# Kernel tuning notes

Hardware: AMD Instinct MI355X
Metric: run time of the kernel (lower is better)

Reference implementation:

```python
import jax, jax.numpy as jnp
import numpy as np

B, T = 64, 2048
ENC, DEC = 512, 1024
CONV, K, HID = 32, 31, 256
PAD = (K - 1) // 2


def setup_inputs() -> dict:
    key = jax.random.key(0)
    ks = jax.random.split(key, 10)
    s = 0.05
    enc_output = jax.random.normal(ks[0], (B, T, ENC), jnp.float32)
    dec_state = jax.random.normal(ks[1], (B, DEC), jnp.float32)
    prev = jax.random.uniform(ks[2], (B, T), jnp.float32)
    prev_att_w = prev / jnp.sum(prev, axis=-1, keepdims=True)
    text_len = jax.random.randint(ks[3], (B,), T // 2, T + 1)
    W_enc = jax.random.normal(ks[4], (HID, ENC), jnp.float32) * s
    b_enc = jnp.zeros((HID,), jnp.float32)
    W_dec = jax.random.normal(ks[5], (HID, DEC), jnp.float32) * s
    W_att = jax.random.normal(ks[6], (HID, CONV), jnp.float32) * s
    conv_w = jax.random.normal(ks[7], (CONV, 1, K), jnp.float32) * s  # (out,in,k)
    w_w = jax.random.normal(ks[8], (1, HID), jnp.float32) * s
    w_b = jnp.zeros((1,), jnp.float32)
    return dict(enc_output=enc_output, dec_state=dec_state, prev_att_w=prev_att_w,
                text_len=text_len, W_enc=W_enc, b_enc=b_enc, W_dec=W_dec,
                W_att=W_att, conv_w=conv_w, w_w=w_w, w_b=w_b)


def reference(enc_output, dec_state, prev_att_w, text_len,
              W_enc, b_enc, W_dec, W_att, conv_w, w_w, w_b):
    # pad mask: True where position is beyond the valid length
    mask = jnp.arange(T)[None, :] >= text_len[:, None]              # (B,T) bool

    # processed_memory = fc_enc(enc_output)
    pm = jnp.einsum('btc,hc->bth', enc_output, W_enc) + b_enc       # (B,T,HID)

    # location conv over previous attention weights (same-padding 1D conv)
    conv = jax.lax.conv_general_dilated(
        prev_att_w[:, None, :], conv_w, window_strides=(1,),
        padding=[(PAD, PAD)], dimension_numbers=('NCH', 'OIH', 'NCH'))  # (B,CONV,T)
    att_conv = jnp.einsum('bct,hc->bth', conv, W_att)               # (B,T,HID)

    dec = (dec_state @ W_dec.T)[:, None, :]                         # (B,1,HID)

    energy = jnp.einsum('bth,oh->bto', jnp.tanh(att_conv + pm + dec), w_w)[..., 0] + w_b[0]
    energy = jnp.where(mask, -jnp.inf, energy)                      # masked fill
    att_w = jax.nn.softmax(energy, axis=1)                          # (B,T)
    att_c = jnp.einsum('btc,bt->bc', enc_output, att_w)             # (B,ENC)
    return att_c, att_w
```

## Files before the change

### kernel.cpp

```cpp
#include <hip/hip_runtime.h>
#include <hip/hip_bf16.h>

#define NB   64
#define NT   2048
#define NENC 512
#define NDEC 1024
#define NCONV 32
#define NK   31
#define NHID 256
#define NPAD 15

typedef __attribute__((ext_vector_type(8))) short bf16x8;
typedef __attribute__((ext_vector_type(4))) float f32x4;

#define WS_WSW 0
#define WS_GSW 262144
#define WS_DEC 278528

__device__ __forceinline__ short f2b(float f) {
  unsigned u = __builtin_bit_cast(unsigned, f);
  u += 0x7FFFu + ((u >> 16) & 1u);
  return (short)(u >> 16);
}

__global__ __launch_bounds__(256) void prep_kernel(
    const float* __restrict__ W_enc, const float* __restrict__ W_att,
    const float* __restrict__ conv_w, const float* __restrict__ dec_state,
    const float* __restrict__ W_dec, char* __restrict__ ws)
{
  const int tid = threadIdx.x;
  const int blk = blockIdx.x;
  if (blk < 512) {
    int idx = blk * 256 + tid;
    int j = idx & 7, lane = (idx >> 3) & 63;
    int ks = (idx >> 9) & 15, nt = idx >> 13;
    int h = nt * 16 + (lane & 15);
    int k = ks * 32 + (lane >> 4) * 8 + j;
    ((short*)(ws + WS_WSW))[idx] = f2b(W_enc[h * NENC + k]);
  } else if (blk < 544) {
    int idx = (blk - 512) * 256 + tid;
    int j = idx & 7, lane = (idx >> 3) & 63, nt = idx >> 9;
    int h = nt * 16 + (lane & 15);
    int k = (lane >> 4) * 8 + j;
    float v = 0.f;
    if (k < NK) {
      for (int c = 0; c < NCONV; ++c)
        v += W_att[h * NCONV + c] * conv_w[c * NK + k];
    }
    ((short*)(ws + WS_GSW))[idx] = f2b(v);
  } else {
    int idx = (blk - 544) * 256 + tid;
    int h = idx & 255, b = idx >> 8;
    const float4* ds4 = (const float4*)(dec_state + b * NDEC);
    const float4* wd4 = (const float4*)(W_dec + h * NDEC);
    float s = 0.f;
    for (int d = 0; d < NDEC / 4; ++d) {
      float4 a = ds4[d], w = wd4[d];
      s += a.x * w.x + a.y * w.y + a.z * w.z + a.w * w.w;
    }
    ((float*)(ws + WS_DEC))[idx] = s;
  }
}

__global__ __launch_bounds__(256, 2) void energy_kernel(
    const float* __restrict__ enc, const float* __restrict__ prev,
    const int* __restrict__ text_len, const float* __restrict__ b_enc,
    const float* __restrict__ w_w, const float* __restrict__ w_b,
    const char* __restrict__ ws, float* __restrict__ e_out)
{
  const int b = blockIdx.y;
  const int t0 = blockIdx.x * 64;
  if (t0 >= text_len[b]) return;

  __shared__ short As[64][512];

  const int tid = threadIdx.x;
  const int wave = tid >> 6, lane = tid & 63;
  const int col = lane & 15, quad = lane >> 4;

  const short* Wsw = (const short*)(ws + WS_WSW);
  const short* Gsw = (const short*)(ws + WS_GSW);
  const float* dec_proj = (const float*)(ws + WS_DEC);

  f32x4 acc[4][4];
  {
    bf16x8 gf[4];
#pragma unroll
    for (int i = 0; i < 4; ++i)
      gf[i] = ((const bf16x8*)Gsw)[(wave * 4 + i) * 64 + lane];
    const float* pb = prev + b * NT;
#pragma unroll
    for (int mt = 0; mt < 4; ++mt) {
      int t = t0 + mt * 16 + col;
      bf16x8 pf;
#pragma unroll
      for (int j = 0; j < 8; ++j) {
        int k = quad * 8 + j;
        int ti = t + k - NPAD;
        float v = (k < NK && ti >= 0 && ti < NT) ? pb[ti] : 0.f;
        pf[j] = f2b(v);
      }
      f32x4 z = {0.f, 0.f, 0.f, 0.f};
#pragma unroll
      for (int i = 0; i < 4; ++i)
        acc[mt][i] = __builtin_amdgcn_mfma_f32_16x16x32_bf16(pf, gf[i], z, 0, 0, 0);
    }
  }

  {
    const float* src = enc + ((size_t)b * NT + t0) * NENC;
#pragma unroll 4
    for (int it = 0; it < 16; ++it) {
      int cidx = it * 256 + tid;
      int row = cidx >> 6;
      int c   = cidx & 63;
      const float4* p = (const float4*)(src + row * NENC + c * 8);
      float4 v0 = p[0], v1 = p[1];
      bf16x8 o;
      o[0] = f2b(v0.x); o[1] = f2b(v0.y); o[2] = f2b(v0.z); o[3] = f2b(v0.w);
      o[4] = f2b(v1.x); o[5] = f2b(v1.y); o[6] = f2b(v1.z); o[7] = f2b(v1.w);
      int csw = c ^ (row & 7);
      *(bf16x8*)(&As[row][csw * 8]) = o;
    }
  }
  __syncthreads();

#pragma unroll 2
  for (int ks = 0; ks < 16; ++ks) {
    bf16x8 bf[4];
#pragma unroll
    for (int i = 0; i < 4; ++i)
      bf[i] = ((const bf16x8*)Wsw)[((wave * 4 + i) * 16 + ks) * 64 + lane];
#pragma unroll
    for (int mt = 0; mt < 4; ++mt) {
      int row = mt * 16 + col;
      int chunk = (ks * 4 + quad) ^ (row & 7);
      bf16x8 af = *(const bf16x8*)(&As[row][chunk * 8]);
#pragma unroll
      for (int i = 0; i < 4; ++i)
        acc[mt][i] = __builtin_amdgcn_mfma_f32_16x16x32_bf16(af, bf[i], acc[mt][i], 0, 0, 0);
    }
  }

  __syncthreads();
  float* ep = (float*)&As[0][0];

  const float* dpb = dec_proj + b * NHID;
#pragma unroll
  for (int mt = 0; mt < 4; ++mt) {
#pragma unroll
    for (int r = 0; r < 4; ++r) {
      float s = 0.f;
#pragma unroll
      for (int i = 0; i < 4; ++i) {
        int h = (wave * 4 + i) * 16 + col;
        float x = acc[mt][i][r] + dpb[h] + b_enc[h];
        float e2 = __expf(2.f * x);
        s += w_w[h] * ((e2 - 1.f) / (e2 + 1.f));
      }
      s += __shfl_xor(s, 1);
      s += __shfl_xor(s, 2);
      s += __shfl_xor(s, 4);
      s += __shfl_xor(s, 8);
      if (col == 0) ep[wave * 64 + mt * 16 + quad * 4 + r] = s;
    }
  }
  __syncthreads();
  if (tid < 64) {
    float e = ep[tid] + ep[64 + tid] + ep[128 + tid] + ep[192 + tid] + w_b[0];
    e_out[b * NT + t0 + tid] = e;
  }
}

__global__ __launch_bounds__(256) void softmax_kernel(
    const int* __restrict__ text_len, float* __restrict__ d_out)
{
  const int b = blockIdx.x, tid = threadIdx.x;
  const int wave = tid >> 6, lane = tid & 63;
  __shared__ float red[4];

  d_out[b * NENC + tid] = 0.f;
  d_out[b * NENC + tid + 256] = 0.f;

  const int len = text_len[b];
  float* e = d_out + NB * NENC + b * NT;

  float ev[8];
#pragma unroll
  for (int j = 0; j < 8; ++j) ev[j] = e[tid + j * 256];

  float m = -3.0e38f;
#pragma unroll
  for (int j = 0; j < 8; ++j)
    if (tid + j * 256 < len) m = fmaxf(m, ev[j]);
#pragma unroll
  for (int o = 1; o < 64; o <<= 1) m = fmaxf(m, __shfl_xor(m, o));
  if (lane == 0) red[wave] = m;
  __syncthreads();
  m = fmaxf(fmaxf(red[0], red[1]), fmaxf(red[2], red[3]));
  __syncthreads();

  float p[8], sum = 0.f;
#pragma unroll
  for (int j = 0; j < 8; ++j) {
    p[j] = (tid + j * 256 < len) ? __expf(ev[j] - m) : 0.f;
    sum += p[j];
  }
#pragma unroll
  for (int o = 1; o < 64; o <<= 1) sum += __shfl_xor(sum, o);
  if (lane == 0) red[wave] = sum;
  __syncthreads();
  sum = red[0] + red[1] + red[2] + red[3];
  float inv = 1.f / sum;
#pragma unroll
  for (int j = 0; j < 8; ++j) e[tid + j * 256] = p[j] * inv;
}

__global__ __launch_bounds__(128) void context_kernel(
    const float* __restrict__ enc, const int* __restrict__ text_len,
    float* __restrict__ d_out)
{
  const int b = blockIdx.y;
  const int ts = blockIdx.x * 64;
  const int len = text_len[b];
  if (ts >= len) return;
  const int n = min(64, len - ts);
  const float* aw = d_out + NB * NENC + b * NT + ts;
  const float* ebase = enc + ((size_t)b * NT + ts) * NENC + threadIdx.x * 4;
  float4 acc = {0.f, 0.f, 0.f, 0.f};
  for (int t = 0; t < n; ++t) {
    float w = aw[t];
    float4 v = *(const float4*)(ebase + (size_t)t * NENC);
    acc.x += w * v.x; acc.y += w * v.y; acc.z += w * v.z; acc.w += w * v.w;
  }
  float* oc = d_out + b * NENC + threadIdx.x * 4;
  atomicAdd(oc + 0, acc.x);
  atomicAdd(oc + 1, acc.y);
  atomicAdd(oc + 2, acc.z);
  atomicAdd(oc + 3, acc.w);
}

extern "C" void kernel_launch(void* const* d_in, const int* in_sizes, int n_in,
                              void* d_out, int out_size, void* d_ws, size_t ws_size,
                              hipStream_t stream)
{
  const float* enc      = (const float*)d_in[0];
  const float* dec_st   = (const float*)d_in[1];
  const float* prev     = (const float*)d_in[2];
  const int*   text_len = (const int*)d_in[3];
  const float* W_enc    = (const float*)d_in[4];
  const float* b_enc    = (const float*)d_in[5];
  const float* W_dec    = (const float*)d_in[6];
  const float* W_att    = (const float*)d_in[7];
  const float* conv_w   = (const float*)d_in[8];
  const float* w_w      = (const float*)d_in[9];
  const float* w_b      = (const float*)d_in[10];
  float* out = (float*)d_out;
  char* ws = (char*)d_ws;

  hipLaunchKernelGGL(prep_kernel, dim3(608), dim3(256), 0, stream,
                     W_enc, W_att, conv_w, dec_st, W_dec, ws);
  hipLaunchKernelGGL(energy_kernel, dim3(32, 64), dim3(256), 0, stream,
                     enc, prev, text_len, b_enc, w_w, w_b, ws, out + NB * NENC);
  hipLaunchKernelGGL(softmax_kernel, dim3(64), dim3(256), 0, stream,
                     text_len, out);
  hipLaunchKernelGGL(context_kernel, dim3(32, 64), dim3(128), 0, stream,
                     enc, text_len, out);
}
```

Measured before the change: 489.7 us.

## Fuse context reduction into energy kernel with flash-style split softmax

Computes per-tile softmax partials (max and sum) and a partial context vector inside the energy kernel. It reuses the bf16 encoder tile already staged in shared memory, so the separate context kernel's second full read of enc_output and its atomics go away. A new finalize kernel merges the per-tile partials, writes the context, and normalizes the attention weights. It also prefetches the next W_enc fragment in the MFMA loop, splits the decoder projection dot product across 4 lanes, and simplifies tanh. The context is now accumulated from bf16-rounded encoder values, which lowers its precision.

Measured after the change: 431.7 us. 1.13x faster.

```diff
diff --git a/kernel.cpp b/kernel.cpp
--- a/kernel.cpp
+++ b/kernel.cpp
@@ -16,11 +16,19 @@
 #define WS_WSW 0
 #define WS_GSW 262144
 #define WS_DEC 278528
+#define WS_CTX 344064
+#define WS_ML  4538368
 
 __device__ __forceinline__ short f2b(float f) {
   unsigned u = __builtin_bit_cast(unsigned, f);
   u += 0x7FFFu + ((u >> 16) & 1u);
   return (short)(u >> 16);
+}
+__device__ __forceinline__ float blo(unsigned u) {
+  return __builtin_bit_cast(float, u << 16);
+}
+__device__ __forceinline__ float bhi(unsigned u) {
+  return __builtin_bit_cast(float, u & 0xFFFF0000u);
 }
 
 __global__ __launch_bounds__(256) void prep_kernel(
@@ -50,15 +58,19 @@
     ((short*)(ws + WS_GSW))[idx] = f2b(v);
   } else {
     int idx = (blk - 544) * 256 + tid;
-    int h = idx & 255, b = idx >> 8;
-    const float4* ds4 = (const float4*)(dec_state + b * NDEC);
-    const float4* wd4 = (const float4*)(W_dec + h * NDEC);
+    int bh = idx >> 2, q = idx & 3;
+    int h = bh & 255, bb = bh >> 8;
+    const float4* ds4 = (const float4*)(dec_state + bb * NDEC + q * 256);
+    const float4* wd4 = (const float4*)(W_dec + h * NDEC + q * 256);
     float s = 0.f;
-    for (int d = 0; d < NDEC / 4; ++d) {
+#pragma unroll 8
+    for (int d = 0; d < 64; ++d) {
       float4 a = ds4[d], w = wd4[d];
       s += a.x * w.x + a.y * w.y + a.z * w.z + a.w * w.w;
     }
-    ((float*)(ws + WS_DEC))[idx] = s;
+    s += __shfl_xor(s, 1);
+    s += __shfl_xor(s, 2);
+    if (q == 0) ((float*)(ws + WS_DEC))[bh] = s;
   }
 }
 
@@ -66,11 +78,13 @@
     const float* __restrict__ enc, const float* __restrict__ prev,
     const int* __restrict__ text_len, const float* __restrict__ b_enc,
     const float* __restrict__ w_w, const float* __restrict__ w_b,
-    const char* __restrict__ ws, float* __restrict__ e_out)
+    char* __restrict__ ws, float* __restrict__ e_out)
 {
   const int b = blockIdx.y;
-  const int t0 = blockIdx.x * 64;
-  if (t0 >= text_len[b]) return;
+  const int bx = blockIdx.x;
+  const int t0 = bx * 64;
+  const int len = text_len[b];
+  if (t0 >= len) return;
 
   __shared__ short As[64][512];
 
@@ -125,12 +139,17 @@
   }
   __syncthreads();
 
+  bf16x8 bcur[4];
+#pragma unroll
+  for (int i = 0; i < 4; ++i)
+    bcur[i] = ((const bf16x8*)Wsw)[((wave * 4 + i) * 16 + 0) * 64 + lane];
 #pragma unroll 2
   for (int ks = 0; ks < 16; ++ks) {
-    bf16x8 bf[4];
+    bf16x8 bnxt[4];
+    int ksn = (ks + 1) & 15;
 #pragma unroll
     for (int i = 0; i < 4; ++i)
-      bf[i] = ((const bf16x8*)Wsw)[((wave * 4 + i) * 16 + ks) * 64 + lane];
+      bnxt[i] = ((const bf16x8*)Wsw)[((wave * 4 + i) * 16 + ksn) * 64 + lane];
 #pragma unroll
     for (int mt = 0; mt < 4; ++mt) {
       int row = mt * 16 + col;
@@ -138,14 +157,27 @@
       bf16x8 af = *(const bf16x8*)(&As[row][chunk * 8]);
 #pragma unroll
       for (int i = 0; i < 4; ++i)
-        acc[mt][i] = __builtin_amdgcn_mfma_f32_16x16x32_bf16(af, bf[i], acc[mt][i], 0, 0, 0);
-    }
-  }
-
-  __syncthreads();
+        acc[mt][i] = __builtin_amdgcn_mfma_f32_16x16x32_bf16(af, bcur[i], acc[mt][i], 0, 0, 0);
+    }
+#pragma unroll
+    for (int i = 0; i < 4; ++i) bcur[i] = bnxt[i];
+  }
+
+  __syncthreads();
+  unsigned sv = ((const unsigned*)As)[tid];
+  __syncthreads();
+
   float* ep = (float*)&As[0][0];
+  float* wwp = (float*)&As[0][0];
 
   const float* dpb = dec_proj + b * NHID;
+  float pre[4], wv[4];
+#pragma unroll
+  for (int i = 0; i < 4; ++i) {
+    int h = (wave * 4 + i) * 16 + col;
+    pre[i] = dpb[h] + b_enc[h];
+    wv[i] = w_w[h];
+  }
 #pragma unroll
   for (int mt = 0; mt < 4; ++mt) {
 #pragma unroll
@@ -153,10 +185,9 @@
       float s = 0.f;
 #pragma unroll
       for (int i = 0; i < 4; ++i) {
-        int h = (wave * 4 + i) * 16 + col;
-        float x = acc[mt][i][r] + dpb[h] + b_enc[h];
+        float x = acc[mt][i][r] + pre[i];
         float e2 = __expf(2.f * x);
-        s += w_w[h] * ((e2 - 1.f) / (e2 + 1.f));
+        s += wv[i] * (1.f - 2.f / (e2 + 1.f));
       }
       s += __shfl_xor(s, 1);
       s += __shfl_xor(s, 2);
@@ -166,78 +197,91 @@
     }
   }
   __syncthreads();
+
   if (tid < 64) {
     float e = ep[tid] + ep[64 + tid] + ep[128 + tid] + ep[192 + tid] + w_b[0];
     e_out[b * NT + t0 + tid] = e;
-  }
-}
-
-__global__ __launch_bounds__(256) void softmax_kernel(
-    const int* __restrict__ text_len, float* __restrict__ d_out)
+    float me = (t0 + tid < len) ? e : -3.0e38f;
+    float m = me;
+#pragma unroll
+    for (int o = 1; o < 64; o <<= 1) m = fmaxf(m, __shfl_xor(m, o));
+    float w = __expf(me - m);
+    wwp[tid] = w;
+    float l = w;
+#pragma unroll
+    for (int o = 1; o < 64; o <<= 1) l += __shfl_xor(l, o);
+    if (tid == 0) {
+      float* ml = (float*)(ws + WS_ML) + (b * 32 + bx) * 2;
+      ml[0] = m; ml[1] = l;
+    }
+  }
+  __syncthreads();
+
+  {
+    const int c0 = tid * 2;
+    const int chunk = c0 >> 3, oc = c0 & 7;
+    float w0 = wwp[0];
+    float a0 = w0 * blo(sv);
+    float a1 = w0 * bhi(sv);
+#pragma unroll 7
+    for (int t = 1; t < 64; ++t) {
+      float w = wwp[t];
+      unsigned u = *(const unsigned*)(&As[t][((chunk ^ (t & 7)) << 3) + oc]);
+      a0 += w * blo(u);
+      a1 += w * bhi(u);
+    }
+    float2 st = {a0, a1};
+    *(float2*)((float*)(ws + WS_CTX) + (size_t)(b * 32 + bx) * NENC + c0) = st;
+  }
+}
+
+__global__ __launch_bounds__(256) void finalize_kernel(
+    const int* __restrict__ text_len, const char* __restrict__ ws,
+    float* __restrict__ d_out)
 {
   const int b = blockIdx.x, tid = threadIdx.x;
-  const int wave = tid >> 6, lane = tid & 63;
-  __shared__ float red[4];
-
-  d_out[b * NENC + tid] = 0.f;
-  d_out[b * NENC + tid + 256] = 0.f;
-
   const int len = text_len[b];
-  float* e = d_out + NB * NENC + b * NT;
-
-  float ev[8];
-#pragma unroll
-  for (int j = 0; j < 8; ++j) ev[j] = e[tid + j * 256];
-
-  float m = -3.0e38f;
-#pragma unroll
-  for (int j = 0; j < 8; ++j)
-    if (tid + j * 256 < len) m = fmaxf(m, ev[j]);
-#pragma unroll
-  for (int o = 1; o < 64; o <<= 1) m = fmaxf(m, __shfl_xor(m, o));
-  if (lane == 0) red[wave] = m;
-  __syncthreads();
-  m = fmaxf(fmaxf(red[0], red[1]), fmaxf(red[2], red[3]));
-  __syncthreads();
-
-  float p[8], sum = 0.f;
+  const int nv = (len + 63) >> 6;
+  __shared__ float sc[32];
+  __shared__ float sml[2];
+
+  if (tid < 64) {
+    const float* ml = (const float*)(ws + WS_ML) + b * 64;
+    float mi = -3.0e38f, li = 0.f;
+    if (tid < nv) { mi = ml[tid * 2]; li = ml[tid * 2 + 1]; }
+    float m = mi;
+#pragma unroll
+    for (int o = 1; o < 64; o <<= 1) m = fmaxf(m, __shfl_xor(m, o));
+    float e = __expf(mi - m);
+    float l = li * e;
+#pragma unroll
+    for (int o = 1; o < 64; o <<= 1) l += __shfl_xor(l, o);
+    if (tid < 32) sc[tid] = e;
+    if (tid == 0) { sml[0] = m; sml[1] = l; }
+  }
+  __syncthreads();
+  const float m = sml[0], invl = 1.f / sml[1];
+
+  {
+    const float* ctx = (const float*)(ws + WS_CTX) + (size_t)b * 32 * NENC;
+    float a0 = 0.f, a1 = 0.f;
+    for (int i = 0; i < nv; ++i) {
+      float s = sc[i];
+      a0 += s * ctx[i * NENC + tid];
+      a1 += s * ctx[i * NENC + tid + 256];
+    }
+    d_out[b * NENC + tid] = a0 * invl;
+    d_out[b * NENC + tid + 256] = a1 * invl;
+  }
+
+  float* aw = d_out + NB * NENC + b * NT;
 #pragma unroll
   for (int j = 0; j < 8; ++j) {
-    p[j] = (tid + j * 256 < len) ? __expf(ev[j] - m) : 0.f;
-    sum += p[j];
-  }
-#pragma unroll
-  for (int o = 1; o < 64; o <<= 1) sum += __shfl_xor(sum, o);
-  if (lane == 0) red[wave] = sum;
-  __syncthreads();
-  sum = red[0] + red[1] + red[2] + red[3];
-  float inv = 1.f / sum;
-#pragma unroll
-  for (int j = 0; j < 8; ++j) e[tid + j * 256] = p[j] * inv;
-}
-
-__global__ __launch_bounds__(128) void context_kernel(
-    const float* __restrict__ enc, const int* __restrict__ text_len,
-    float* __restrict__ d_out)
-{
-  const int b = blockIdx.y;
-  const int ts = blockIdx.x * 64;
-  const int len = text_len[b];
-  if (ts >= len) return;
-  const int n = min(64, len - ts);
-  const float* aw = d_out + NB * NENC + b * NT + ts;
-  const float* ebase = enc + ((size_t)b * NT + ts) * NENC + threadIdx.x * 4;
-  float4 acc = {0.f, 0.f, 0.f, 0.f};
-  for (int t = 0; t < n; ++t) {
-    float w = aw[t];
-    float4 v = *(const float4*)(ebase + (size_t)t * NENC);
-    acc.x += w * v.x; acc.y += w * v.y; acc.z += w * v.z; acc.w += w * v.w;
-  }
-  float* oc = d_out + b * NENC + threadIdx.x * 4;
-  atomicAdd(oc + 0, acc.x);
-  atomicAdd(oc + 1, acc.y);
-  atomicAdd(oc + 2, acc.z);
-  atomicAdd(oc + 3, acc.w);
+    int t = tid + j * 256;
+    float v = 0.f;
+    if (t < len) v = __expf(aw[t] - m) * invl;
+    aw[t] = v;
+  }
 }
 
 extern "C" void kernel_launch(void* const* d_in, const int* in_sizes, int n_in,
@@ -258,12 +302,10 @@
   float* out = (float*)d_out;
   char* ws = (char*)d_ws;
 
-  hipLaunchKernelGGL(prep_kernel, dim3(608), dim3(256), 0, stream,
+  hipLaunchKernelGGL(prep_kernel, dim3(800), dim3(256), 0, stream,
                      W_enc, W_att, conv_w, dec_st, W_dec, ws);
   hipLaunchKernelGGL(energy_kernel, dim3(32, 64), dim3(256), 0, stream,
                      enc, prev, text_len, b_enc, w_w, w_b, ws, out + NB * NENC);
-  hipLaunchKernelGGL(softmax_kernel, dim3(64), dim3(256), 0, stream,
-                     text_len, out);
-  hipLaunchKernelGGL(context_kernel, dim3(32, 64), dim3(128), 0, stream,
-                     enc, text_len, out);
-}
+  hipLaunchKernelGGL(finalize_kernel, dim3(64), dim3(256), 0, stream,
+                     text_len, ws, out);
+}
```
